# Kernel tuning notes

Hardware: AMD Instinct MI355X
Metric: run time of the kernel (lower is better)

The kernel has to match this reference:

```python
import jax, jax.numpy as jnp
import numpy as np

IMG_H, IMG_W = 800, 1216   # input image size (stride-32 backbone)
FH, FW = 25, 38            # feature map spatial dims
C = 2048                   # feature channels (100352 = 2048*7*7)
N_BOXES = 2000             # RPN proposals
N_KEEP = 8                 # hard-coded `for i in range(0, 8)` in source
NMS_THRESH = 0.6


def _pairwise_iou(box, boxes):
    # box [4] vs boxes [N,4], corner (x1,y1,x2,y2) format, torchvision convention
    ix1 = jnp.maximum(box[0], boxes[:, 0])
    iy1 = jnp.maximum(box[1], boxes[:, 1])
    ix2 = jnp.minimum(box[2], boxes[:, 2])
    iy2 = jnp.minimum(box[3], boxes[:, 3])
    inter = jnp.clip(ix2 - ix1, 0.0) * jnp.clip(iy2 - iy1, 0.0)
    a1 = (box[2] - box[0]) * (box[3] - box[1])
    a2 = (boxes[:, 2] - boxes[:, 0]) * (boxes[:, 3] - boxes[:, 1])
    return inter / (a1 + a2 - inter)


def _adaptive_maxpool_roi(feat, x, y, w, h):
    # feat [C,FH,FW]; pool window rows [y, y+h), cols [x, x+w) down to 7x7
    # PyTorch AdaptiveMaxPool2d: cell i covers [floor(i*h/7), ceil((i+1)*h/7))
    i = jnp.arange(7)
    r0 = y + (i * h) // 7
    r1 = y + ((i + 1) * h + 6) // 7
    c0 = x + (i * w) // 7
    c1 = x + ((i + 1) * w + 6) // 7
    rows = jnp.arange(feat.shape[1])
    cols = jnp.arange(feat.shape[2])
    rmask = (rows[None, :] >= r0[:, None]) & (rows[None, :] < r1[:, None])  # [7,FH]
    cmask = (cols[None, :] >= c0[:, None]) & (cols[None, :] < c1[:, None])  # [7,FW]
    # row reduce: [C,7,FW], then col reduce: [C,7,7]
    t = jnp.where(rmask[None, :, :, None], feat[:, None, :, :], -jnp.inf).max(axis=2)
    out = jnp.where(cmask[None, None, :, :], t[:, :, None, :], -jnp.inf).max(axis=3)
    return out


def setup_inputs() -> dict:
    key = jax.random.key(0)
    ks = jax.random.split(key, 12)
    feat_map = jax.random.normal(ks[0], (1, C, FH, FW), dtype=jnp.float32)
    # proposals fully inside the image (so index_inside keeps them)
    x1 = jax.random.uniform(ks[1], (N_BOXES,), minval=0.0, maxval=IMG_W - 256.0)
    y1 = jax.random.uniform(ks[2], (N_BOXES,), minval=0.0, maxval=IMG_H - 256.0)
    bw = jax.random.uniform(ks[3], (N_BOXES,), minval=16.0, maxval=256.0)
    bh = jax.random.uniform(ks[4], (N_BOXES,), minval=16.0, maxval=256.0)
    rois = jnp.stack([x1, y1, x1 + bw, y1 + bh], axis=1).astype(jnp.float32)
    scores = jax.random.uniform(ks[5], (N_BOXES, 2), dtype=jnp.float32)
    s = 0.01  # nn.init.normal_(w, 0, 0.01)
    return {
        "feat_map": feat_map,
        "rois": rois,
        "scores": scores,
        "w1": jax.random.normal(ks[6], (4096, 100352), dtype=jnp.float32) * s,
        "b1": jnp.zeros((4096,), jnp.float32),
        "w2": jax.random.normal(ks[7], (4096, 4096), dtype=jnp.float32) * s,
        "b2": jnp.zeros((4096,), jnp.float32),
        "wc": jax.random.normal(ks[8], (81, 4096), dtype=jnp.float32) * s,
        "bc": jnp.zeros((81,), jnp.float32),
        "wl": jax.random.normal(ks[9], (324, 4096), dtype=jnp.float32) * s,
        "bl": jnp.zeros((324,), jnp.float32),
    }


def reference(feat_map, rois, scores, w1, b1, w2, b2, wc, bc, wl, bl):
    feat = feat_map[0]  # [C,FH,FW]
    # index_inside filter
    valid = (rois[:, 0] >= 0) & (rois[:, 1] >= 0) & (rois[:, 2] <= IMG_W) & (rois[:, 3] <= IMG_H)
    fg = scores[:, 1]
    # greedy NMS: first N_KEEP survivors at IoU 0.6 == torchvision.ops.nms(...)[:8]
    alive = valid
    sels = []
    for _ in range(N_KEEP):
        m = jnp.where(alive, fg, -jnp.inf)
        s = jnp.argmax(m)
        sels.append(s)
        iou = _pairwise_iou(rois[s], rois)
        alive = alive & (iou <= NMS_THRESH)
    sels = jnp.stack(sels)
    b = rois[sels] / 32.0  # [8,4]
    # faithful to source: x,y,w,h = int(x+0.5), int(y+0.5), int(w+1), int(h+1)
    x = jnp.floor(b[:, 0] + 0.5).astype(jnp.int32)
    y = jnp.floor(b[:, 1] + 0.5).astype(jnp.int32)
    w = jnp.floor(b[:, 2] + 1.0).astype(jnp.int32)
    h = jnp.floor(b[:, 3] + 1.0).astype(jnp.int32)
    bad = (x < 0) | (x >= FW) | (y < 0) | (y >= FH) | (w < 1) | (x + w > FW) | (h < 1) | (y + h > FH)
    # fallback: pool the entire feature map (roi = feat_map[0])
    x = jnp.where(bad, 0, x)
    y = jnp.where(bad, 0, y)
    w = jnp.where(bad, FW, w)
    h = jnp.where(bad, FH, h)
    pooled = jax.vmap(lambda xx, yy, ww, hh: _adaptive_maxpool_roi(feat, xx, yy, ww, hh))(x, y, w, h)  # [8,C,7,7]
    flat = pooled.reshape(N_KEEP, -1)  # [8,100352]
    o = flat @ w1.T + b1   # no activation in the original
    o = o @ w2.T + b2
    roi_scores = o @ wc.T + bc  # [8,81]
    roi_locs = o @ wl.T + bl    # [8,324]
    return jnp.concatenate([roi_scores, roi_locs], axis=-1)  # [8,405]
```

## Files before the change

### kernel.cpp

```cpp
#include <hip/hip_runtime.h>
#include <cstddef>
#include <math.h>

#define IMG_H 800
#define IMG_W 1216
#define FH 25
#define FWW 38
#define CC 2048
#define NBOX 2000
#define NKEEP 8
#define D1 100352
#define K1 4096
#define NSLICE 16
#define DPS (D1/NSLICE)

__global__ __launch_bounds__(256) void nms_sel_kernel(const float* __restrict__ rois,
                                                      const float* __restrict__ scores,
                                                      int* __restrict__ roi_out) {
    __shared__ float4 s_box[NBOX];
    __shared__ float  s_fg[NBOX];
    __shared__ float  red_v[256];
    __shared__ int    red_i[256];
    __shared__ int    s_sels[NKEEP];
    const int tid = threadIdx.x;

    for (int i = tid; i < NBOX; i += 256) {
        float x1 = rois[i*4+0], y1 = rois[i*4+1], x2 = rois[i*4+2], y2 = rois[i*4+3];
        s_box[i] = make_float4(x1, y1, x2, y2);
        bool valid = (x1 >= 0.f) && (y1 >= 0.f) && (x2 <= (float)IMG_W) && (y2 <= (float)IMG_H);
        s_fg[i] = valid ? scores[i*2+1] : -INFINITY;
    }
    __syncthreads();

    for (int it = 0; it < NKEEP; ++it) {
        float bv = -INFINITY; int bi = NBOX;
        for (int i = tid; i < NBOX; i += 256) {
            float v = s_fg[i];
            if (v > bv || (v == bv && i < bi)) { bv = v; bi = i; }
        }
        red_v[tid] = bv; red_i[tid] = bi;
        __syncthreads();
        for (int off = 128; off > 0; off >>= 1) {
            if (tid < off) {
                float v = red_v[tid+off]; int ii = red_i[tid+off];
                if (v > red_v[tid] || (v == red_v[tid] && ii < red_i[tid])) {
                    red_v[tid] = v; red_i[tid] = ii;
                }
            }
            __syncthreads();
        }
        int s = red_i[0];
        if (s >= NBOX) s = 0;
        if (tid == 0) s_sels[it] = s;

        float4 bs = s_box[s];
        float a1 = (bs.z - bs.x) * (bs.w - bs.y);
        for (int i = tid; i < NBOX; i += 256) {
            float4 b = s_box[i];
            float ix1 = fmaxf(bs.x, b.x), iy1 = fmaxf(bs.y, b.y);
            float ix2 = fminf(bs.z, b.z), iy2 = fminf(bs.w, b.w);
            float inter = fmaxf(ix2 - ix1, 0.f) * fmaxf(iy2 - iy1, 0.f);
            float a2 = (b.z - b.x) * (b.w - b.y);
            float iou = inter / (a1 + a2 - inter);
            if (!(iou <= 0.6f)) s_fg[i] = -INFINITY;
        }
        __syncthreads();
    }

    if (tid < NKEEP) {
        int s = s_sels[tid];
        float4 b = s_box[s];
        int x = (int)floorf(b.x / 32.0f + 0.5f);
        int y = (int)floorf(b.y / 32.0f + 0.5f);
        int w = (int)floorf(b.z / 32.0f + 1.0f);
        int h = (int)floorf(b.w / 32.0f + 1.0f);
        bool bad = (x < 0) || (x >= FWW) || (y < 0) || (y >= FH) ||
                   (w < 1) || (x + w > FWW) || (h < 1) || (y + h > FH);
        if (bad) { x = 0; y = 0; w = FWW; h = FH; }
        roi_out[tid*4+0] = x; roi_out[tid*4+1] = y;
        roi_out[tid*4+2] = w; roi_out[tid*4+3] = h;
    }
}

__global__ __launch_bounds__(256) void roi_pool_kernel(const float* __restrict__ feat,
                                                       const int* __restrict__ roi_out,
                                                       float* __restrict__ pooled) {
    int idx = blockIdx.x * 256 + threadIdx.x;
    if (idx >= NKEEP * D1) return;
    int r    = idx / D1;
    int rem  = idx - r * D1;
    int c    = rem / 49;
    int cell = rem - c * 49;
    int i = cell / 7;
    int j = cell - i * 7;
    int x = roi_out[r*4+0], y = roi_out[r*4+1], w = roi_out[r*4+2], h = roi_out[r*4+3];
    int r0 = y + (i * h) / 7;
    int r1 = y + ((i + 1) * h + 6) / 7;
    int c0 = x + (j * w) / 7;
    int c1 = x + ((j + 1) * w + 6) / 7;
    const float* fc = feat + (size_t)c * (FH * FWW);
    float m = -INFINITY;
    for (int rr = r0; rr < r1; ++rr) {
        const float* fr = fc + rr * FWW;
        for (int cc2 = c0; cc2 < c1; ++cc2) m = fmaxf(m, fr[cc2]);
    }
    pooled[idx] = m;
}

__global__ __launch_bounds__(256) void init_bias8_kernel(const float* __restrict__ b,
                                                         float* __restrict__ o, int K) {
    int i = blockIdx.x * 256 + threadIdx.x;
    if (i < NKEEP * K) o[i] = b[i & (K - 1)];
}

__global__ __launch_bounds__(256) void fc1_kernel(const float* __restrict__ w1,
                                                  const float* __restrict__ flat,
                                                  float* __restrict__ o1) {
    const int kb = blockIdx.x >> 4;
    const int ds = blockIdx.x & 15;
    const int tid = threadIdx.x;
    const int kq = tid >> 4;
    const int dl = tid & 15;
    const int k0 = kb * 64 + kq * 4;
    const int dbase = ds * DPS + dl * 4;

    const float* wp0 = w1 + (size_t)k0 * D1 + dbase;
    const float* wp1 = wp0 + D1;
    const float* wp2 = wp1 + D1;
    const float* wp3 = wp2 + D1;
    const float* fp  = flat + dbase;

    float acc[4][8];
    #pragma unroll
    for (int a = 0; a < 4; ++a)
        #pragma unroll
        for (int n = 0; n < 8; ++n) acc[a][n] = 0.f;

    for (int itn = 0; itn < DPS / 64; ++itn) {
        const int off = itn * 64;
        float4 wv0 = *(const float4*)(wp0 + off);
        float4 wv1 = *(const float4*)(wp1 + off);
        float4 wv2 = *(const float4*)(wp2 + off);
        float4 wv3 = *(const float4*)(wp3 + off);
        #pragma unroll
        for (int n = 0; n < 8; ++n) {
            float4 f = *(const float4*)(fp + (size_t)n * D1 + off);
            acc[0][n] += wv0.x*f.x + wv0.y*f.y + wv0.z*f.z + wv0.w*f.w;
            acc[1][n] += wv1.x*f.x + wv1.y*f.y + wv1.z*f.z + wv1.w*f.w;
            acc[2][n] += wv2.x*f.x + wv2.y*f.y + wv2.z*f.z + wv2.w*f.w;
            acc[3][n] += wv3.x*f.x + wv3.y*f.y + wv3.z*f.z + wv3.w*f.w;
        }
    }

    #pragma unroll
    for (int a = 0; a < 4; ++a) {
        #pragma unroll
        for (int n = 0; n < 8; ++n) {
            float v = acc[a][n];
            v += __shfl_xor(v, 1);
            v += __shfl_xor(v, 2);
            v += __shfl_xor(v, 4);
            v += __shfl_xor(v, 8);
            if (dl == 0) atomicAdd(&o1[n * K1 + k0 + a], v);
        }
    }
}

__global__ __launch_bounds__(256) void fc2_kernel(const float* __restrict__ w2,
                                                  const float* __restrict__ o1,
                                                  const float* __restrict__ b2,
                                                  float* __restrict__ o2) {
    int gw   = (blockIdx.x * 256 + threadIdx.x) >> 6;
    int lane = threadIdx.x & 63;
    if (gw >= K1) return;
    const float4* wr = (const float4*)(w2 + (size_t)gw * K1);
    const float4* fo = (const float4*)o1;
    float acc[8];
    #pragma unroll
    for (int n = 0; n < 8; ++n) acc[n] = 0.f;
    for (int itn = 0; itn < K1 / 256; ++itn) {
        float4 wv = wr[itn * 64 + lane];
        #pragma unroll
        for (int n = 0; n < 8; ++n) {
            float4 f = fo[n * (K1/4) + itn * 64 + lane];
            acc[n] += wv.x*f.x + wv.y*f.y + wv.z*f.z + wv.w*f.w;
        }
    }
    #pragma unroll
    for (int n = 0; n < 8; ++n) {
        float v = acc[n];
        #pragma unroll
        for (int m = 32; m >= 1; m >>= 1) v += __shfl_xor(v, m);
        if (lane == 0) o2[n * K1 + gw] = v + b2[gw];
    }
}

__global__ __launch_bounds__(256) void fc3_kernel(const float* __restrict__ wc,
                                                  const float* __restrict__ bc,
                                                  const float* __restrict__ wl,
                                                  const float* __restrict__ bl,
                                                  const float* __restrict__ o2,
                                                  float* __restrict__ out) {
    int gw   = (blockIdx.x * 256 + threadIdx.x) >> 6;
    int lane = threadIdx.x & 63;
    if (gw >= 405) return;
    const float* wrow; float bias;
    if (gw < 81) { wrow = wc + (size_t)gw * K1;        bias = bc[gw]; }
    else         { wrow = wl + (size_t)(gw - 81) * K1; bias = bl[gw - 81]; }
    const float4* wr = (const float4*)wrow;
    const float4* fo = (const float4*)o2;
    float acc[8];
    #pragma unroll
    for (int n = 0; n < 8; ++n) acc[n] = 0.f;
    for (int itn = 0; itn < K1 / 256; ++itn) {
        float4 wv = wr[itn * 64 + lane];
        #pragma unroll
        for (int n = 0; n < 8; ++n) {
            float4 f = fo[n * (K1/4) + itn * 64 + lane];
            acc[n] += wv.x*f.x + wv.y*f.y + wv.z*f.z + wv.w*f.w;
        }
    }
    #pragma unroll
    for (int n = 0; n < 8; ++n) {
        float v = acc[n];
        #pragma unroll
        for (int m = 32; m >= 1; m >>= 1) v += __shfl_xor(v, m);
        if (lane == 0) out[n * 405 + gw] = v + bias;
    }
}

extern "C" void kernel_launch(void* const* d_in, const int* in_sizes, int n_in,
                              void* d_out, int out_size, void* d_ws, size_t ws_size,
                              hipStream_t stream) {
    const float* feat   = (const float*)d_in[0];
    const float* rois   = (const float*)d_in[1];
    const float* scores = (const float*)d_in[2];
    const float* w1     = (const float*)d_in[3];
    const float* b1     = (const float*)d_in[4];
    const float* w2     = (const float*)d_in[5];
    const float* b2     = (const float*)d_in[6];
    const float* wc     = (const float*)d_in[7];
    const float* bc     = (const float*)d_in[8];
    const float* wl     = (const float*)d_in[9];
    const float* bl     = (const float*)d_in[10];
    float* out = (float*)d_out;

    int*   roi_out = (int*)d_ws;
    float* pooled  = (float*)d_ws + 256;
    float* o1      = pooled + (size_t)NKEEP * D1;
    float* o2      = o1 + NKEEP * K1;

    nms_sel_kernel<<<1, 256, 0, stream>>>(rois, scores, roi_out);
    roi_pool_kernel<<<(NKEEP * D1 + 255) / 256, 256, 0, stream>>>(feat, roi_out, pooled);
    init_bias8_kernel<<<(NKEEP * K1 + 255) / 256, 256, 0, stream>>>(b1, o1, K1);
    fc1_kernel<<<64 * NSLICE, 256, 0, stream>>>(w1, pooled, o1);
    fc2_kernel<<<K1 / 4, 256, 0, stream>>>(w2, o1, b2, o2);
    fc3_kernel<<<(405 * 64 + 255) / 256, 256, 0, stream>>>(wc, bc, wl, bl, o2, out);
}
```

Baseline: 416.3 us.

## Transpose pooled features and software-pipeline streamed fc1 weights with nontemporal loads

The ROI pool output is stored interleaved by ROI ([D][8] instead of [8][D]), so fc1 reads all eight ROI values for a feature chunk as contiguous vectors. fc1 now double-buffers its weight loads (prefetching the next chunk while computing the current one) and uses nontemporal loads for the 1.6 GB w1 stream, with a launch-bounds occupancy hint. fc2 and fc3 also switch to nontemporal weight loads. The aim is to keep the weight stream, which dominates the runtime, closer to HBM bandwidth without polluting the cache. The cost is more registers and some added code complexity.

After: 589.5 us. +41.6%, slower.

```diff
diff --git a/kernel.cpp b/kernel.cpp
--- a/kernel.cpp
+++ b/kernel.cpp
@@ -1,18 +1,23 @@
 #include <hip/hip_runtime.h>
 #include <cstddef>
 #include <math.h>
+
+typedef float v4 __attribute__((ext_vector_type(4)));
 
 #define IMG_H 800
 #define IMG_W 1216
 #define FH 25
 #define FWW 38
-#define CC 2048
 #define NBOX 2000
 #define NKEEP 8
 #define D1 100352
 #define K1 4096
 #define NSLICE 16
 #define DPS (D1/NSLICE)
+
+__device__ inline v4 ldnt4(const float* p) {
+    return __builtin_nontemporal_load((const v4*)p);
+}
 
 __global__ __launch_bounds__(256) void nms_sel_kernel(const float* __restrict__ rois,
                                                       const float* __restrict__ scores,
@@ -84,13 +89,13 @@
 
 __global__ __launch_bounds__(256) void roi_pool_kernel(const float* __restrict__ feat,
                                                        const int* __restrict__ roi_out,
-                                                       float* __restrict__ pooled) {
+                                                       float* __restrict__ flat_t) {
     int idx = blockIdx.x * 256 + threadIdx.x;
     if (idx >= NKEEP * D1) return;
-    int r    = idx / D1;
-    int rem  = idx - r * D1;
-    int c    = rem / 49;
-    int cell = rem - c * 49;
+    int r = idx & 7;
+    int d = idx >> 3;
+    int c = d / 49;
+    int cell = d - c * 49;
     int i = cell / 7;
     int j = cell - i * 7;
     int x = roi_out[r*4+0], y = roi_out[r*4+1], w = roi_out[r*4+2], h = roi_out[r*4+3];
@@ -104,7 +109,7 @@
         const float* fr = fc + rr * FWW;
         for (int cc2 = c0; cc2 < c1; ++cc2) m = fmaxf(m, fr[cc2]);
     }
-    pooled[idx] = m;
+    flat_t[idx] = m;
 }
 
 __global__ __launch_bounds__(256) void init_bias8_kernel(const float* __restrict__ b,
@@ -113,9 +118,9 @@
     if (i < NKEEP * K) o[i] = b[i & (K - 1)];
 }
 
-__global__ __launch_bounds__(256) void fc1_kernel(const float* __restrict__ w1,
-                                                  const float* __restrict__ flat,
-                                                  float* __restrict__ o1) {
+__global__ __launch_bounds__(256, 4) void fc1_kernel(const float* __restrict__ w1,
+                                                     const float* __restrict__ flat_t,
+                                                     float* __restrict__ o1) {
     const int kb = blockIdx.x >> 4;
     const int ds = blockIdx.x & 15;
     const int tid = threadIdx.x;
@@ -124,11 +129,8 @@
     const int k0 = kb * 64 + kq * 4;
     const int dbase = ds * DPS + dl * 4;
 
-    const float* wp0 = w1 + (size_t)k0 * D1 + dbase;
-    const float* wp1 = wp0 + D1;
-    const float* wp2 = wp1 + D1;
-    const float* wp3 = wp2 + D1;
-    const float* fp  = flat + dbase;
+    const float* wp = w1 + (size_t)k0 * D1 + dbase;
+    const float* ft = flat_t + (size_t)dbase * 8;
 
     float acc[4][8];
     #pragma unroll
@@ -136,20 +138,44 @@
         #pragma unroll
         for (int n = 0; n < 8; ++n) acc[a][n] = 0.f;
 
-    for (int itn = 0; itn < DPS / 64; ++itn) {
-        const int off = itn * 64;
-        float4 wv0 = *(const float4*)(wp0 + off);
-        float4 wv1 = *(const float4*)(wp1 + off);
-        float4 wv2 = *(const float4*)(wp2 + off);
-        float4 wv3 = *(const float4*)(wp3 + off);
-        #pragma unroll
-        for (int n = 0; n < 8; ++n) {
-            float4 f = *(const float4*)(fp + (size_t)n * D1 + off);
-            acc[0][n] += wv0.x*f.x + wv0.y*f.y + wv0.z*f.z + wv0.w*f.w;
-            acc[1][n] += wv1.x*f.x + wv1.y*f.y + wv1.z*f.z + wv1.w*f.w;
-            acc[2][n] += wv2.x*f.x + wv2.y*f.y + wv2.z*f.z + wv2.w*f.w;
-            acc[3][n] += wv3.x*f.x + wv3.y*f.y + wv3.z*f.z + wv3.w*f.w;
-        }
+    v4 wa[4], wb[4], fv[8];
+    #pragma unroll
+    for (int a = 0; a < 4; ++a) wa[a] = ldnt4(wp + (size_t)a * D1);
+
+#define FC1_FMA(W)                                              \
+    _Pragma("unroll")                                           \
+    for (int j = 0; j < 8; ++j) {                               \
+        _Pragma("unroll")                                       \
+        for (int a = 0; a < 4; ++a) {                           \
+            acc[a][(j&1)*4+0] += W[a][j>>1] * fv[j][0];         \
+            acc[a][(j&1)*4+1] += W[a][j>>1] * fv[j][1];         \
+            acc[a][(j&1)*4+2] += W[a][j>>1] * fv[j][2];         \
+            acc[a][(j&1)*4+3] += W[a][j>>1] * fv[j][3];         \
+        }                                                       \
+    }
+
+    for (int i2 = 0; i2 < 49; ++i2) {
+        const int offA = i2 * 128;
+        const int offB = offA + 64;
+        const int offN = (i2 < 48) ? (offA + 128) : 0;
+
+        #pragma unroll
+        for (int a = 0; a < 4; ++a) wb[a] = ldnt4(wp + (size_t)a * D1 + offB);
+        {
+            const v4* fp = (const v4*)(ft + (size_t)offA * 8);
+            #pragma unroll
+            for (int j = 0; j < 8; ++j) fv[j] = fp[j];
+        }
+        FC1_FMA(wa);
+
+        #pragma unroll
+        for (int a = 0; a < 4; ++a) wa[a] = ldnt4(wp + (size_t)a * D1 + offN);
+        {
+            const v4* fp = (const v4*)(ft + (size_t)offB * 8);
+            #pragma unroll
+            for (int j = 0; j < 8; ++j) fv[j] = fp[j];
+        }
+        FC1_FMA(wb);
     }
 
     #pragma unroll
@@ -173,17 +199,17 @@
     int gw   = (blockIdx.x * 256 + threadIdx.x) >> 6;
     int lane = threadIdx.x & 63;
     if (gw >= K1) return;
-    const float4* wr = (const float4*)(w2 + (size_t)gw * K1);
-    const float4* fo = (const float4*)o1;
+    const float* wr = w2 + (size_t)gw * K1;
+    const v4* fo = (const v4*)o1;
     float acc[8];
     #pragma unroll
     for (int n = 0; n < 8; ++n) acc[n] = 0.f;
     for (int itn = 0; itn < K1 / 256; ++itn) {
-        float4 wv = wr[itn * 64 + lane];
+        v4 wv = ldnt4(wr + (itn * 64 + lane) * 4);
         #pragma unroll
         for (int n = 0; n < 8; ++n) {
-            float4 f = fo[n * (K1/4) + itn * 64 + lane];
-            acc[n] += wv.x*f.x + wv.y*f.y + wv.z*f.z + wv.w*f.w;
+            v4 f = fo[n * (K1/4) + itn * 64 + lane];
+            acc[n] += wv[0]*f[0] + wv[1]*f[1] + wv[2]*f[2] + wv[3]*f[3];
         }
     }
     #pragma unroll
@@ -207,17 +233,16 @@
     const float* wrow; float bias;
     if (gw < 81) { wrow = wc + (size_t)gw * K1;        bias = bc[gw]; }
     else         { wrow = wl + (size_t)(gw - 81) * K1; bias = bl[gw - 81]; }
-    const float4* wr = (const float4*)wrow;
-    const float4* fo = (const float4*)o2;
+    const v4* fo = (const v4*)o2;
     float acc[8];
     #pragma unroll
     for (int n = 0; n < 8; ++n) acc[n] = 0.f;
     for (int itn = 0; itn < K1 / 256; ++itn) {
-        float4 wv = wr[itn * 64 + lane];
+        v4 wv = ldnt4(wrow + (itn * 64 + lane) * 4);
         #pragma unroll
         for (int n = 0; n < 8; ++n) {
-            float4 f = fo[n * (K1/4) + itn * 64 + lane];
-            acc[n] += wv.x*f.x + wv.y*f.y + wv.z*f.z + wv.w*f.w;
+            v4 f = fo[n * (K1/4) + itn * 64 + lane];
+            acc[n] += wv[0]*f[0] + wv[1]*f[1] + wv[2]*f[2] + wv[3]*f[3];
         }
     }
     #pragma unroll
@@ -246,14 +271,14 @@
     float* out = (float*)d_out;
 
     int*   roi_out = (int*)d_ws;
-    float* pooled  = (float*)d_ws + 256;
-    float* o1      = pooled + (size_t)NKEEP * D1;
+    float* flat_t  = (float*)d_ws + 256;
+    float* o1      = flat_t + (size_t)NKEEP * D1;
     float* o2      = o1 + NKEEP * K1;
 
     nms_sel_kernel<<<1, 256, 0, stream>>>(rois, scores, roi_out);
-    roi_pool_kernel<<<(NKEEP * D1 + 255) / 256, 256, 0, stream>>>(feat, roi_out, pooled);
+    roi_pool_kernel<<<(NKEEP * D1 + 255) / 256, 256, 0, stream>>>(feat, roi_out, flat_t);
     init_bias8_kernel<<<(NKEEP * K1 + 255) / 256, 256, 0, stream>>>(b1, o1, K1);
-    fc1_kernel<<<64 * NSLICE, 256, 0, stream>>>(w1, pooled, o1);
+    fc1_kernel<<<64 * NSLICE, 256, 0, stream>>>(w1, flat_t, o1);
     fc2_kernel<<<K1 / 4, 256, 0, stream>>>(w2, o1, b2, o2);
     fc3_kernel<<<(405 * 64 + 255) / 256, 256, 0, stream>>>(wc, bc, wl, bl, o2, out);
 }
```

## Stage flat activations in shared memory and split fc1 reduction into more slices

Applied to the files above, without the earlier changes.

The fc1 kernel now copies the eight activation rows for its D slice into LDS once per block and reads them from shared memory inside the inner loop, instead of reloading them from global memory in every thread. The D dimension is split into 98 slices of 1024 instead of 16 large slices, so far more blocks are launched, giving better parallelism over the 1.6 GB weight stream. The costs are more atomicAdds into the output (98 partial sums per element) and a sync plus 32 KB of LDS per block, which may limit occupancy.

After: 495.8 us. 1.19x slower.

```diff
diff --git a/kernel.cpp b/kernel.cpp
--- a/kernel.cpp
+++ b/kernel.cpp
@@ -1,18 +1,19 @@
 #include <hip/hip_runtime.h>
 #include <cstddef>
 #include <math.h>
+
+typedef float v4 __attribute__((ext_vector_type(4)));
 
 #define IMG_H 800
 #define IMG_W 1216
 #define FH 25
 #define FWW 38
-#define CC 2048
 #define NBOX 2000
 #define NKEEP 8
 #define D1 100352
 #define K1 4096
-#define NSLICE 16
-#define DPS (D1/NSLICE)
+#define NSLICE 98
+#define DPS 1024
 
 __global__ __launch_bounds__(256) void nms_sel_kernel(const float* __restrict__ rois,
                                                       const float* __restrict__ scores,
@@ -116,19 +117,31 @@
 __global__ __launch_bounds__(256) void fc1_kernel(const float* __restrict__ w1,
                                                   const float* __restrict__ flat,
                                                   float* __restrict__ o1) {
-    const int kb = blockIdx.x >> 4;
-    const int ds = blockIdx.x & 15;
+    __shared__ float s_f[NKEEP][DPS];
+
+    const int bid = blockIdx.x;
+    const int kb = bid / NSLICE;
+    const int ds = bid - kb * NSLICE;
     const int tid = threadIdx.x;
     const int kq = tid >> 4;
     const int dl = tid & 15;
     const int k0 = kb * 64 + kq * 4;
-    const int dbase = ds * DPS + dl * 4;
-
-    const float* wp0 = w1 + (size_t)k0 * D1 + dbase;
-    const float* wp1 = wp0 + D1;
-    const float* wp2 = wp1 + D1;
-    const float* wp3 = wp2 + D1;
-    const float* fp  = flat + dbase;
+    const int dbase = ds * DPS;
+
+    {
+        const v4* src = (const v4*)(flat);
+        v4* dst = (v4*)&s_f[0][0];
+        #pragma unroll
+        for (int it = 0; it < (NKEEP * DPS / 4) / 256; ++it) {
+            int l = it * 256 + tid;
+            int n  = l >> 8;
+            int d4 = l & 255;
+            dst[l] = src[(size_t)n * (D1 / 4) + (dbase >> 2) + d4];
+        }
+    }
+    __syncthreads();
+
+    const float* wp = w1 + (size_t)k0 * D1 + dbase + dl * 4;
 
     float acc[4][8];
     #pragma unroll
@@ -138,17 +151,17 @@
 
     for (int itn = 0; itn < DPS / 64; ++itn) {
         const int off = itn * 64;
-        float4 wv0 = *(const float4*)(wp0 + off);
-        float4 wv1 = *(const float4*)(wp1 + off);
-        float4 wv2 = *(const float4*)(wp2 + off);
-        float4 wv3 = *(const float4*)(wp3 + off);
-        #pragma unroll
-        for (int n = 0; n < 8; ++n) {
-            float4 f = *(const float4*)(fp + (size_t)n * D1 + off);
-            acc[0][n] += wv0.x*f.x + wv0.y*f.y + wv0.z*f.z + wv0.w*f.w;
-            acc[1][n] += wv1.x*f.x + wv1.y*f.y + wv1.z*f.z + wv1.w*f.w;
-            acc[2][n] += wv2.x*f.x + wv2.y*f.y + wv2.z*f.z + wv2.w*f.w;
-            acc[3][n] += wv3.x*f.x + wv3.y*f.y + wv3.z*f.z + wv3.w*f.w;
+        v4 wv0 = *(const v4*)(wp + off);
+        v4 wv1 = *(const v4*)(wp + (size_t)D1 + off);
+        v4 wv2 = *(const v4*)(wp + (size_t)2 * D1 + off);
+        v4 wv3 = *(const v4*)(wp + (size_t)3 * D1 + off);
+        #pragma unroll
+        for (int n = 0; n < 8; ++n) {
+            v4 f = *(const v4*)&s_f[n][dl * 4 + off];
+            acc[0][n] += wv0[0]*f[0] + wv0[1]*f[1] + wv0[2]*f[2] + wv0[3]*f[3];
+            acc[1][n] += wv1[0]*f[0] + wv1[1]*f[1] + wv1[2]*f[2] + wv1[3]*f[3];
+            acc[2][n] += wv2[0]*f[0] + wv2[1]*f[1] + wv2[2]*f[2] + wv2[3]*f[3];
+            acc[3][n] += wv3[0]*f[0] + wv3[1]*f[1] + wv3[2]*f[2] + wv3[3]*f[3];
         }
     }
 
```
